# Optimization experiments

Measured on AMD Instinct MI355X. Metric: run time of the kernel, lower is better.

The kernel has to match this reference:

```python
import jax, jax.numpy as jnp
import numpy as np


def setup_inputs() -> dict:
    key = jax.random.key(0)
    ks = jax.random.split(key, 4)
    B, S, D, H, E = 2, 2048, 1024, 4096, 8
    scale_in = 1.0 / np.sqrt(D)
    scale_h = 1.0 / np.sqrt(H)
    return {
        "x": jax.random.normal(ks[0], (B, S, D), dtype=jnp.float32),
        "Wr": jax.random.normal(ks[1], (E, D), dtype=jnp.float32) * scale_in,
        "br": jnp.zeros((E,), dtype=jnp.float32),
        "W1": jax.random.normal(ks[2], (E, H, D), dtype=jnp.float32) * scale_in,
        "b1": jnp.zeros((E, H), dtype=jnp.float32),
        "W2": jax.random.normal(ks[3], (E, D, H), dtype=jnp.float32) * scale_h,
        "b2": jnp.zeros((E, D), dtype=jnp.float32),
        "top_k": 2,
    }


def reference(x, Wr, br, W1, b1, W2, b2, top_k):
    B, S, D = x.shape
    E = Wr.shape[0]
    x_flat = x.reshape(-1, D)                                   # [N, D]
    # Router: top-k logits, softmax over the selected k values only
    logits = x_flat @ Wr.T + br                                 # [N, E]
    top_vals, top_idx = jax.lax.top_k(logits, top_k)            # [N, k]
    gates = jax.nn.softmax(top_vals, axis=-1)                   # [N, k]
    # Per-expert combine weight: gate_e[n, e] = sum_k gates[n, k] * 1[top_idx[n,k]==e]
    gate_e = jnp.einsum("nk,nke->ne", gates,
                        jax.nn.one_hot(top_idx, E, dtype=x.dtype))  # [N, E]
    # Dense all-expert MLP (grouped GEMM), then masked combine. Same math as
    # the per-expert gather/scatter loop: unselected experts get zero gate.
    h = jax.nn.relu(jnp.einsum("nd,ehd->neh", x_flat, W1) + b1)     # [N, E, H]
    y = jnp.einsum("neh,edh->ned", h, W2) + b2                      # [N, E, D]
    out = jnp.einsum("ned,ne->nd", y, gate_e)                       # [N, D]
    return out.reshape(B, S, D)
```

## Files before the change

### kernel.cpp

```cpp
#include <hip/hip_runtime.h>
#include <hip/hip_bf16.h>
#include <stdint.h>

#define N_TOK 4096
#define D_ 1024
#define H_ 4096
#define E_ 8
#define NSLOT (N_TOK*2)
#define BM 128
#define BN 128
#define BK 32
#define MAXT 72

typedef __attribute__((ext_vector_type(8))) short short8;
typedef __attribute__((ext_vector_type(4))) float floatx4;
typedef unsigned int u32;

__device__ __forceinline__ unsigned short f2bf(float f){
    union { float f; unsigned int u; } c; c.f = f;
    unsigned int u = c.u;
    unsigned int r = (u + 0x7fffu + ((u >> 16) & 1u)) >> 16;
    return (unsigned short)r;
}

__device__ __forceinline__ void async16(const void* g, void* l){
    __builtin_amdgcn_global_load_lds(
        (const __attribute__((address_space(1))) u32*)g,
        (__attribute__((address_space(3))) u32*)l, 16, 0, 0);
}

__global__ __launch_bounds__(256) void router_kernel(
    const float* __restrict__ x, const float* __restrict__ Wr,
    const float* __restrict__ br, int* __restrict__ topIdx,
    float* __restrict__ topGate)
{
    int n = blockIdx.x * 4 + (threadIdx.x >> 6);
    int lane = threadIdx.x & 63;
    const float4* xp = (const float4*)(x + (size_t)n * D_);
    float acc[E_];
#pragma unroll
    for (int e = 0; e < E_; e++) acc[e] = 0.f;
#pragma unroll
    for (int j = 0; j < 4; j++){
        int idx = j * 64 + lane;
        float4 xv = xp[idx];
#pragma unroll
        for (int e = 0; e < E_; e++){
            float4 wv = ((const float4*)(Wr + (size_t)e * D_))[idx];
            acc[e] += xv.x*wv.x + xv.y*wv.y + xv.z*wv.z + xv.w*wv.w;
        }
    }
#pragma unroll
    for (int e = 0; e < E_; e++){
        float v = acc[e];
        for (int off = 32; off > 0; off >>= 1) v += __shfl_xor(v, off, 64);
        acc[e] = v;
    }
    if (lane == 0){
        float best = -1e30f, second = -1e30f; int bi = 0, si = 0;
#pragma unroll
        for (int e = 0; e < E_; e++){
            float v = acc[e] + br[e];
            if (v > best){ second = best; si = bi; best = v; bi = e; }
            else if (v > second){ second = v; si = e; }
        }
        float e1 = __expf(second - best);
        float denom = 1.f + e1;
        topIdx[n*2+0] = bi;  topIdx[n*2+1] = si;
        topGate[n*2+0] = 1.f/denom;  topGate[n*2+1] = e1/denom;
    }
}

__global__ __launch_bounds__(256) void hist_kernel(
    const int* __restrict__ topIdx, int* __restrict__ hdr)
{
    __shared__ int c[E_];
    int t = threadIdx.x;
    if (t < E_) c[t] = 0;
    __syncthreads();
    int e = topIdx[blockIdx.x * 256 + t];
    atomicAdd(&c[e], 1);
    __syncthreads();
    if (t < E_) hdr[256 + blockIdx.x * E_ + t] = c[t];
}

__global__ __launch_bounds__(64) void scan2_kernel(int* __restrict__ hdr)
{
    __shared__ int cnt[32 * E_];
    __shared__ int tot[E_];
    __shared__ int offs[E_ + 1];
    int t = threadIdx.x;
    for (int i = t; i < 32 * E_; i += 64) cnt[i] = hdr[256 + i];
    __syncthreads();
    if (t < E_){
        int s = 0;
        for (int b = 0; b < 32; b++) s += cnt[b * E_ + t];
        tot[t] = s;
    }
    __syncthreads();
    if (t == 0){
        int o = 0;
        for (int e = 0; e < E_; e++){ offs[e] = o; o += tot[e]; }
        offs[E_] = o;
    }
    __syncthreads();
    if (t < E_ + 1) hdr[16 + t] = offs[t];
    if (t < E_){
        int run = offs[t];
        for (int b = 0; b < 32; b++){ hdr[512 + b * E_ + t] = run; run += cnt[b * E_ + t]; }
    }
    if (t == 0){
        int tn = 0;
        for (int e = 0; e < E_; e++){
            int nt = (tot[e] + BM - 1) >> 7;
            for (int i = 0; i < nt; i++){ hdr[32 + tn] = e; hdr[112 + tn] = offs[e] + (i << 7); tn++; }
        }
        for (; tn < MAXT; tn++){ hdr[32 + tn] = -1; hdr[112 + tn] = 0; }
    }
}

__global__ __launch_bounds__(256) void pos_kernel(
    const int* __restrict__ topIdx, const float* __restrict__ topGate,
    const int* __restrict__ hdr, int* __restrict__ posOf,
    int* __restrict__ rowTok, float* __restrict__ rowGate)
{
    __shared__ int c[E_];
    int t = threadIdx.x;
    if (t < E_) c[t] = 0;
    __syncthreads();
    int slot = blockIdx.x * 256 + t;
    int e = topIdx[slot];
    int r = atomicAdd(&c[e], 1);
    int pos = hdr[512 + blockIdx.x * E_ + e] + r;
    posOf[slot] = pos;
    rowTok[pos] = slot >> 1;
    rowGate[pos] = topGate[slot];
}

__global__ __launch_bounds__(256) void copy_kernel(
    const float* __restrict__ x, const int* __restrict__ posOf,
    unsigned short* __restrict__ xg)
{
    int slot = blockIdx.x * 4 + (threadIdx.x >> 6);
    int lane = threadIdx.x & 63;
    int n = slot >> 1;
    int pos = posOf[slot];
    const float4* xp = (const float4*)(x + (size_t)n * D_);
    ushort4* op = (ushort4*)(xg + (size_t)pos * D_);
#pragma unroll
    for (int j = 0; j < 4; j++){
        float4 v = xp[j * 64 + lane];
        ushort4 o; o.x=f2bf(v.x); o.y=f2bf(v.y); o.z=f2bf(v.z); o.w=f2bf(v.w);
        op[j * 64 + lane] = o;
    }
}

template<int MODE>
__global__ __launch_bounds__(256) void moe_gemm(
    const unsigned short* __restrict__ A, int Ktot,
    const float* __restrict__ Wbase, size_t wStride,
    const float* __restrict__ biasBase, int biasStride,
    const int* __restrict__ hdr,
    const int* __restrict__ rowTok, const float* __restrict__ rowGate,
    unsigned short* __restrict__ hout, float* __restrict__ out)
{
    int gid = blockIdx.y * gridDim.x + blockIdx.x;
    int per = gridDim.x * 8;
    int g = gid / per, rr = gid % per;
    int by = g * 8 + (rr & 7);
    int bx = rr >> 3;

    int e = hdr[32 + bx];
    if (e < 0) return;
    int rowBase = hdr[112 + bx];
    int validRows = hdr[16 + e + 1] - rowBase;

    int kChunk = Ktot / gridDim.z;
    int kStart = blockIdx.z * kChunk;
    int nIter  = kChunk / BK;

    __shared__ __align__(16) unsigned short As[2][BM * BK];
    __shared__ __align__(16) float          BsF[2][BN * BK];

    const float* biasE = biasBase + (size_t)e * biasStride + by * BN;

    const int tid  = threadIdx.x;
    const int lane = tid & 63, wave = tid >> 6;
    const int wm = wave & 1, wn = wave >> 1;
    const int l16 = lane & 15, quad = lane >> 4;

    const float* Wexp = Wbase + (size_t)e * wStride + (size_t)(by * BN) * Ktot;

    size_t aOff[2]; int aS[2];
#pragma unroll
    for (int i = 0; i < 2; i++){
        int s = i * 256 + tid;
        int r = s >> 2, gst = s & 3;
        int gsrc = gst ^ ((r >> 1) & 3);
        int ar = rowBase + r;
        ar = ar < (NSLOT - 1) ? ar : (NSLOT - 1);
        aOff[i] = (size_t)ar * Ktot + gsrc * 8;
        aS[i] = s * 16;
    }
    size_t bOff[4]; int bS[4];
#pragma unroll
    for (int i = 0; i < 4; i++){
        int s = i * 256 + tid;
        int r = s >> 3, c = s & 7;
        bOff[i] = (size_t)r * Ktot + (size_t)((c ^ (r & 7)) * 4);
        bS[i] = s * 16;
    }

    floatx4 acc[4][4];
#pragma unroll
    for (int mi = 0; mi < 4; mi++)
#pragma unroll
        for (int ni = 0; ni < 4; ni++)
            acc[mi][ni] = (floatx4){0.f,0.f,0.f,0.f};

#pragma unroll
    for (int i = 0; i < 2; i++)
        async16(A + aOff[i] + kStart, (char*)As[0] + aS[i]);
#pragma unroll
    for (int i = 0; i < 4; i++)
        async16(Wexp + bOff[i] + kStart, (char*)BsF[0] + bS[i]);

    for (int it = 0; it < nIter; it++){
        __syncthreads();
        int p = it & 1;
        if (it + 1 < nIter){
            int kn = kStart + (it + 1) * BK;
#pragma unroll
            for (int i = 0; i < 2; i++)
                async16(A + aOff[i] + kn, (char*)As[p ^ 1] + aS[i]);
#pragma unroll
            for (int i = 0; i < 4; i++)
                async16(Wexp + bOff[i] + kn, (char*)BsF[p ^ 1] + bS[i]);
        }
        short8 af[4], bfr[4];
#pragma unroll
        for (int mi = 0; mi < 4; mi++){
            int r = wm*64 + mi*16 + l16;
            int gq = quad ^ ((r >> 1) & 3);
            af[mi] = *(const short8*)(As[p] + r * BK + gq * 8);
        }
#pragma unroll
        for (int ni = 0; ni < 4; ni++){
            int n = wn*64 + ni*16 + l16;
            int g0 = (2*quad)     ^ (n & 7);
            int g1 = (2*quad + 1) ^ (n & 7);
            float4 u0 = *(const float4*)(BsF[p] + n * BK + g0 * 4);
            float4 u1 = *(const float4*)(BsF[p] + n * BK + g1 * 4);
            union { short8 s; __hip_bfloat162 h[4]; } u;
            u.h[0] = __float22bfloat162_rn(make_float2(u0.x, u0.y));
            u.h[1] = __float22bfloat162_rn(make_float2(u0.z, u0.w));
            u.h[2] = __float22bfloat162_rn(make_float2(u1.x, u1.y));
            u.h[3] = __float22bfloat162_rn(make_float2(u1.z, u1.w));
            bfr[ni] = u.s;
        }
        __builtin_amdgcn_s_setprio(1);
#pragma unroll
        for (int mi = 0; mi < 4; mi++)
#pragma unroll
            for (int ni = 0; ni < 4; ni++)
                acc[mi][ni] = __builtin_amdgcn_mfma_f32_16x16x32_bf16(
                    af[mi], bfr[ni], acc[mi][ni], 0, 0, 0);
        __builtin_amdgcn_s_setprio(0);
    }

    bool addB = (MODE == 1) || (blockIdx.z == 0);
#pragma unroll
    for (int mi = 0; mi < 4; mi++){
#pragma unroll
        for (int r = 0; r < 4; r++){
            int rl = wm*64 + mi*16 + quad*4 + r;
            if (rl >= validRows) continue;
            int grow = rowBase + rl;
            int   tok  = 0;
            float gate = 0.f;
            if (MODE == 2){ tok = rowTok[grow]; gate = rowGate[grow]; }
#pragma unroll
            for (int ni = 0; ni < 4; ni++){
                int lcol = wn*64 + ni*16 + l16;
                int gcol = by * BN + lcol;
                float v = acc[mi][ni][r] + (addB ? biasE[lcol] : 0.f);
                if (MODE == 1){
                    v = v > 0.f ? v : 0.f;
                    hout[(size_t)grow * H_ + gcol] = f2bf(v);
                } else {
                    atomicAdd(out + (size_t)tok * D_ + gcol, gate * v);
                }
            }
        }
    }
}

extern "C" void kernel_launch(void* const* d_in, const int* in_sizes, int n_in,
                              void* d_out, int out_size, void* d_ws, size_t ws_size,
                              hipStream_t stream)
{
    (void)in_sizes; (void)n_in; (void)ws_size;
    const float* x  = (const float*)d_in[0];
    const float* Wr = (const float*)d_in[1];
    const float* br = (const float*)d_in[2];
    const float* W1 = (const float*)d_in[3];
    const float* b1 = (const float*)d_in[4];
    const float* W2 = (const float*)d_in[5];
    const float* b2 = (const float*)d_in[6];
    float* out = (float*)d_out;

    char* ws = (char*)d_ws;
    int*   hdr     = (int*)ws;
    int*   topIdx  = (int*)  (ws + 4096);
    float* topGate = (float*)(ws + 36864);
    int*   posOf   = (int*)  (ws + 69632);
    int*   rowTok  = (int*)  (ws + 102400);
    float* rowGate = (float*)(ws + 135168);
    unsigned short* xg   = (unsigned short*)(ws + 262144);
    unsigned short* hbuf = (unsigned short*)(ws + 17039360);

    hipMemsetAsync(d_out, 0, (size_t)out_size * sizeof(float), stream);

    router_kernel<<<N_TOK/4, 256, 0, stream>>>(x, Wr, br, topIdx, topGate);
    hist_kernel<<<32, 256, 0, stream>>>(topIdx, hdr);
    scan2_kernel<<<1, 64, 0, stream>>>(hdr);
    pos_kernel<<<32, 256, 0, stream>>>(topIdx, topGate, hdr, posOf, rowTok, rowGate);
    copy_kernel<<<NSLOT/4, 256, 0, stream>>>(x, posOf, xg);

    moe_gemm<1><<<dim3(MAXT, H_/BN, 1), 256, 0, stream>>>(
        xg, D_, W1, (size_t)H_ * D_, b1, H_, hdr, rowTok, rowGate, hbuf, nullptr);
    moe_gemm<2><<<dim3(MAXT, D_/BN, 2), 256, 0, stream>>>(
        hbuf, H_, W2, (size_t)D_ * H_, b2, D_, hdr, rowTok, rowGate, nullptr, out);
}
```

Baseline: 632.5 us.

## Convert fp32 weight tile to bf16 once on global load instead of per-wave reads

The fp32 weight tile used to go async straight to shared memory, and each wave converted it to bf16 when reading its MMA fragments. It is now loaded into registers, converted to bf16 once per element, and written to a bf16 shared buffer with the same swizzle as A. This halves B's shared-memory footprint and read traffic and drops the duplicate conversions across waves. The cost is register-staged loads that overlap the MFMAs less freely, and the s_setprio hints are removed.

New measurement: 627.4 us. No clear change (-0.8%).

```diff
diff --git a/kernel.cpp b/kernel.cpp
--- a/kernel.cpp
+++ b/kernel.cpp
@@ -180,7 +180,7 @@
     int nIter  = kChunk / BK;
 
     __shared__ __align__(16) unsigned short As[2][BM * BK];
-    __shared__ __align__(16) float          BsF[2][BN * BK];
+    __shared__ __align__(16) unsigned short Bs[2][BN * BK];
 
     const float* biasE = biasBase + (size_t)e * biasStride + by * BN;
 
@@ -202,13 +202,14 @@
         aOff[i] = (size_t)ar * Ktot + gsrc * 8;
         aS[i] = s * 16;
     }
-    size_t bOff[4]; int bS[4];
-#pragma unroll
-    for (int i = 0; i < 4; i++){
+    const float* bSrc[2]; int bDst[2];
+#pragma unroll
+    for (int i = 0; i < 2; i++){
         int s = i * 256 + tid;
-        int r = s >> 3, c = s & 7;
-        bOff[i] = (size_t)r * Ktot + (size_t)((c ^ (r & 7)) * 4);
-        bS[i] = s * 16;
+        int r = s >> 2, gst = s & 3;
+        int gsrc = gst ^ ((r >> 1) & 3);
+        bSrc[i] = Wexp + (size_t)r * Ktot + gsrc * 8;
+        bDst[i] = s * 16;
     }
 
     floatx4 acc[4][4];
@@ -218,12 +219,28 @@
         for (int ni = 0; ni < 4; ni++)
             acc[mi][ni] = (floatx4){0.f,0.f,0.f,0.f};
 
+    float4 w0a, w0b, w1a, w1b;
+
 #pragma unroll
     for (int i = 0; i < 2; i++)
         async16(A + aOff[i] + kStart, (char*)As[0] + aS[i]);
-#pragma unroll
-    for (int i = 0; i < 4; i++)
-        async16(Wexp + bOff[i] + kStart, (char*)BsF[0] + bS[i]);
+    w0a = *(const float4*)(bSrc[0] + kStart);
+    w0b = *(const float4*)(bSrc[0] + kStart + 4);
+    w1a = *(const float4*)(bSrc[1] + kStart);
+    w1b = *(const float4*)(bSrc[1] + kStart + 4);
+    {
+        union { short8 s; __hip_bfloat162 h[4]; } u;
+        u.h[0] = __float22bfloat162_rn(make_float2(w0a.x, w0a.y));
+        u.h[1] = __float22bfloat162_rn(make_float2(w0a.z, w0a.w));
+        u.h[2] = __float22bfloat162_rn(make_float2(w0b.x, w0b.y));
+        u.h[3] = __float22bfloat162_rn(make_float2(w0b.z, w0b.w));
+        *(short8*)((char*)Bs[0] + bDst[0]) = u.s;
+        u.h[0] = __float22bfloat162_rn(make_float2(w1a.x, w1a.y));
+        u.h[1] = __float22bfloat162_rn(make_float2(w1a.z, w1a.w));
+        u.h[2] = __float22bfloat162_rn(make_float2(w1b.x, w1b.y));
+        u.h[3] = __float22bfloat162_rn(make_float2(w1b.z, w1b.w));
+        *(short8*)((char*)Bs[0] + bDst[1]) = u.s;
+    }
 
     for (int it = 0; it < nIter; it++){
         __syncthreads();
@@ -233,9 +250,10 @@
 #pragma unroll
             for (int i = 0; i < 2; i++)
                 async16(A + aOff[i] + kn, (char*)As[p ^ 1] + aS[i]);
-#pragma unroll
-            for (int i = 0; i < 4; i++)
-                async16(Wexp + bOff[i] + kn, (char*)BsF[p ^ 1] + bS[i]);
+            w0a = *(const float4*)(bSrc[0] + kn);
+            w0b = *(const float4*)(bSrc[0] + kn + 4);
+            w1a = *(const float4*)(bSrc[1] + kn);
+            w1b = *(const float4*)(bSrc[1] + kn + 4);
         }
         short8 af[4], bfr[4];
 #pragma unroll
@@ -247,25 +265,28 @@
 #pragma unroll
         for (int ni = 0; ni < 4; ni++){
             int n = wn*64 + ni*16 + l16;
-            int g0 = (2*quad)     ^ (n & 7);
-            int g1 = (2*quad + 1) ^ (n & 7);
-            float4 u0 = *(const float4*)(BsF[p] + n * BK + g0 * 4);
-            float4 u1 = *(const float4*)(BsF[p] + n * BK + g1 * 4);
-            union { short8 s; __hip_bfloat162 h[4]; } u;
-            u.h[0] = __float22bfloat162_rn(make_float2(u0.x, u0.y));
-            u.h[1] = __float22bfloat162_rn(make_float2(u0.z, u0.w));
-            u.h[2] = __float22bfloat162_rn(make_float2(u1.x, u1.y));
-            u.h[3] = __float22bfloat162_rn(make_float2(u1.z, u1.w));
-            bfr[ni] = u.s;
-        }
-        __builtin_amdgcn_s_setprio(1);
+            int gq = quad ^ ((n >> 1) & 3);
+            bfr[ni] = *(const short8*)(Bs[p] + n * BK + gq * 8);
+        }
 #pragma unroll
         for (int mi = 0; mi < 4; mi++)
 #pragma unroll
             for (int ni = 0; ni < 4; ni++)
                 acc[mi][ni] = __builtin_amdgcn_mfma_f32_16x16x32_bf16(
                     af[mi], bfr[ni], acc[mi][ni], 0, 0, 0);
-        __builtin_amdgcn_s_setprio(0);
+        if (it + 1 < nIter){
+            union { short8 s; __hip_bfloat162 h[4]; } u;
+            u.h[0] = __float22bfloat162_rn(make_float2(w0a.x, w0a.y));
+            u.h[1] = __float22bfloat162_rn(make_float2(w0a.z, w0a.w));
+            u.h[2] = __float22bfloat162_rn(make_float2(w0b.x, w0b.y));
+            u.h[3] = __float22bfloat162_rn(make_float2(w0b.z, w0b.w));
+            *(short8*)((char*)Bs[p ^ 1] + bDst[0]) = u.s;
+            u.h[0] = __float22bfloat162_rn(make_float2(w1a.x, w1a.y));
+            u.h[1] = __float22bfloat162_rn(make_float2(w1a.z, w1a.w));
+            u.h[2] = __float22bfloat162_rn(make_float2(w1b.x, w1b.y));
+            u.h[3] = __float22bfloat162_rn(make_float2(w1b.z, w1b.w));
+            *(short8*)((char*)Bs[p ^ 1] + bDst[1]) = u.s;
+        }
     }
 
     bool addB = (MODE == 1) || (blockIdx.z == 0);
```
